# Kernel optimization log

Hardware: AMD Instinct MI355X
Metric: run time of the kernel (lower is better)

Reference implementation:

```python
import jax, jax.numpy as jnp
import numpy as np

B, N, T_OBS, N_HEAD, D = 4, 2048, 8, 4, 16  # D = t_obs*2 = in/out feat of GAT
S, NSAMP = 2, 20
OUT_DIM = S * NSAMP  # 40
SEG = 64  # pedestrians per scene -> 32 scenes, block-diagonal mask


def _xavier(key, shape, gain=1.414):
    fan_in, fan_out = shape[-2], shape[-1]
    a = gain * np.sqrt(6.0 / (fan_in + fan_out))
    return jax.random.uniform(key, shape, jnp.float32, -a, a)


def setup_inputs() -> dict:
    key = jax.random.key(0)
    ks = jax.random.split(key, 12)
    x = jax.random.normal(ks[0], (B, N, T_OBS, 2), jnp.float32)
    # block-diagonal scene mask: 32 scenes of 64 peds each
    scene_id = jnp.arange(N) // SEG
    mask = (scene_id[:, None] == scene_id[None, :]).astype(jnp.float32)
    w = _xavier(ks[1], (N_HEAD, D, D))
    a_src = _xavier(ks[2], (N_HEAD, D, 1))
    a_dst = _xavier(ks[3], (N_HEAD, D, 1))
    bias = jnp.zeros((D,), jnp.float32)
    # MLP dims: (16,) + (16, 64) + (40,)
    W1 = _xavier(ks[4], (D, 16), gain=1.0)
    b1 = jnp.zeros((16,), jnp.float32)
    W2 = _xavier(ks[5], (16, 64), gain=1.0)
    b2 = jnp.zeros((64,), jnp.float32)
    W3 = _xavier(ks[6], (64, OUT_DIM), gain=1.0)
    b3 = jnp.zeros((OUT_DIM,), jnp.float32)
    return {"x": x, "mask": mask, "w": w, "a_src": a_src, "a_dst": a_dst,
            "bias": bias, "W1": W1, "b1": b1, "W2": W2, "b2": b2, "W3": W3, "b3": b3}


def reference(x, mask, w, a_src, a_dst, bias, W1, b1, W2, b2, W3, b3):
    b, n = x.shape[0], x.shape[1]
    node = x.reshape(b, n, -1)                       # (B, N, 16)
    # GAT
    hp = jnp.einsum('bni,hio->bhno', node, w)        # (B, H, N, D)
    attn_src = jnp.einsum('bhno,hoe->bhne', hp, a_src)[..., 0]  # (B, H, N)
    attn_dst = jnp.einsum('bhno,hoe->bhne', hp, a_dst)[..., 0]  # (B, H, N)
    attn = attn_src[:, :, :, None] * attn_dst[:, :, None, :]    # (B, H, N, N)
    attn = jnp.where(attn >= 0, attn, 0.2 * attn)    # leaky_relu(0.2)
    attn = jax.nn.softmax(attn, axis=-1)             # softmax over full row
    attn = attn * mask                                # mask AFTER softmax (as in source)
    out = jnp.einsum('bhnm,bhmo->bno', attn, hp) + bias
    out = out + hp.sum(axis=1)                        # skip connection
    # MLP head: activation applied BEFORE each Linear (per source), dropout disabled
    y = jax.nn.relu(out) @ W1 + b1
    y = jax.nn.relu(y) @ W2 + b2
    y = jax.nn.relu(y) @ W3 + b3
    y = y.reshape(b, n, NSAMP, -1)[..., 0:S]          # (B, N, 20, 2)
    return jnp.clip(jax.nn.sigmoid(y), 0.01, 0.99)
```

## Files before the change

kernel.cpp:

```cpp
#include <hip/hip_runtime.h>
#include <math.h>

#define L2E 1.4426950408889634f

#if defined(__has_builtin)
#if __has_builtin(__builtin_amdgcn_exp2f)
#define EXP2F(x) __builtin_amdgcn_exp2f(x)
#else
#define EXP2F(x) exp2f(x)
#endif
#else
#define EXP2F(x) exp2f(x)
#endif

#define WS_HP   0
#define WS_S    524288
#define WS_LP   557056
#define WS_LN   589824
#define WS_NME  622592
#define WS_DINV 655360

__global__ __launch_bounds__(128, 4) void k_proj(
    const float* __restrict__ x, const float* __restrict__ w,
    const float* __restrict__ a_src, const float* __restrict__ a_dst,
    float* __restrict__ ws)
{
    __shared__ float w_s[256], as_s[16], ad_s[16];
    int t = threadIdx.x;
    int bh = blockIdx.x >> 5, tile = blockIdx.x & 31;
    int h = bh & 3, b = bh >> 2;
    int nl = t >> 1, half = t & 1;
    int n = tile * 64 + nl;
    w_s[t] = w[h * 256 + t];
    w_s[128 + t] = w[h * 256 + 128 + t];
    if (t < 16) { as_s[t] = a_src[h * 16 + t]; ad_s[t] = a_dst[h * 16 + t]; }
    __syncthreads();

    const float4* xp = (const float4*)(x + ((size_t)b * 2048 + n) * 16);
    float4 x0 = xp[0], x1 = xp[1], x2 = xp[2], x3 = xp[3];
    float nv[16] = {x0.x,x0.y,x0.z,x0.w, x1.x,x1.y,x1.z,x1.w,
                    x2.x,x2.y,x2.z,x2.w, x3.x,x3.y,x3.z,x3.w};
    int ob = half * 8;
    float acc[8];
    #pragma unroll
    for (int o = 0; o < 8; ++o) acc[o] = 0.f;
    #pragma unroll
    for (int i = 0; i < 16; ++i) {
        float ni = nv[i];
        #pragma unroll
        for (int o = 0; o < 8; ++o) acc[o] = fmaf(ni, w_s[i * 16 + ob + o], acc[o]);
    }
    float sv = 0.f, dv = 0.f;
    #pragma unroll
    for (int o = 0; o < 8; ++o) {
        sv = fmaf(acc[o], as_s[ob + o], sv);
        dv = fmaf(acc[o], ad_s[ob + o], dv);
    }
    sv += __shfl_xor(sv, 1);
    dv += __shfl_xor(dv, 1);
    float4* hp4 = (float4*)(ws + WS_HP) + ((size_t)bh * 2048 + n) * 4 + half * 2;
    hp4[0] = make_float4(acc[0], acc[1], acc[2], acc[3]);
    hp4[1] = make_float4(acc[4], acc[5], acc[6], acc[7]);
    if (half == 0) {
        size_t o = (size_t)bh * 2048 + n;
        ws[WS_S + o]  = sv;
        ws[WS_LP + o] = fmaxf(dv, 0.2f * dv);
        ws[WS_LN + o] = fminf(dv, 0.2f * dv);
    }
}

__global__ __launch_bounds__(256, 8) void k_denom(float* __restrict__ ws)
{
    __shared__ __align__(16) float img[4232];
    __shared__ float redmx[4], redmn[4];
    int t = threadIdx.x;
    int bh = blockIdx.x >> 7, tile = blockIdx.x & 127;

    float mx = -3.4e38f, mn = 3.4e38f;
    {
        const float4* glp = (const float4*)(ws + WS_LP) + bh * 512;
        const float4* gln = (const float4*)(ws + WS_LN) + bh * 512;
        #pragma unroll
        for (int k = 0; k < 2; ++k) {
            int j4 = t + k * 256;
            float4 v = glp[j4];
            int pp = j4 >> 5, wi = j4 & 31;
            *(float4*)&img[(pp * 33 + wi) * 4] = v;
            mx = fmaxf(mx, fmaxf(fmaxf(v.x, v.y), fmaxf(v.z, v.w)));
        }
        #pragma unroll
        for (int k = 0; k < 2; ++k) {
            int j4 = t + k * 256;
            float4 v = gln[j4];
            int pp = j4 >> 5, wi = j4 & 31;
            *(float4*)&img[2120 + (pp * 33 + wi) * 4] = v;
            mn = fminf(mn, fminf(fminf(v.x, v.y), fminf(v.z, v.w)));
        }
    }
    #pragma unroll
    for (int off = 32; off >= 1; off >>= 1) {
        mx = fmaxf(mx, __shfl_xor(mx, off));
        mn = fminf(mn, __shfl_xor(mn, off));
    }
    if ((t & 63) == 0) { redmx[t >> 6] = mx; redmn[t >> 6] = mn; }
    __syncthreads();
    float LPmax = fmaxf(fmaxf(redmx[0], redmx[1]), fmaxf(redmx[2], redmx[3]));
    float LNmin = fminf(fminf(redmn[0], redmn[1]), fminf(redmn[2], redmn[3]));

    int r = t >> 4, p = t & 15;
    int grow = tile * 16 + r;
    size_t base = (size_t)bh * 2048 + grow;
    float s = ws[WS_S + base];
    float me_nat = (s >= 0.f) ? s * LPmax : s * LNmin;
    float nme = -me_nat * L2E;
    float sL = s * L2E;
    const float4* ib = (const float4*)&img[(s >= 0.f) ? 0 : 2120] + p * 33;
    float a0 = 0.f, a1 = 0.f, a2 = 0.f, a3 = 0.f;
    #pragma unroll 8
    for (int c4 = 0; c4 < 32; ++c4) {
        float4 v = ib[c4];
        a0 += EXP2F(fmaf(sL, v.x, nme));
        a1 += EXP2F(fmaf(sL, v.y, nme));
        a2 += EXP2F(fmaf(sL, v.z, nme));
        a3 += EXP2F(fmaf(sL, v.w, nme));
    }
    float acc = (a0 + a1) + (a2 + a3);
    acc += __shfl_xor(acc, 1);
    acc += __shfl_xor(acc, 2);
    acc += __shfl_xor(acc, 4);
    acc += __shfl_xor(acc, 8);
    if (p == 0) {
        ws[WS_NME  + base] = nme;
        ws[WS_DINV + base] = 1.0f / acc;
    }
}

__global__ __launch_bounds__(512, 4) void k_scene(
    const float* __restrict__ ws, const float* __restrict__ bias,
    const float* __restrict__ W1, const float* __restrict__ b1,
    const float* __restrict__ W2, const float* __restrict__ b2,
    const float* __restrict__ W3, const float* __restrict__ b3,
    float* __restrict__ out)
{
    __shared__ __align__(16) float RC[5120];
    __shared__ __align__(16) float RB[1024];
    __shared__ __align__(16) float wS[3960];
    __shared__ __align__(16) float imgS[2][4][64];
    __shared__ float feat[16][17];

    const int t = threadIdx.x;
    const int b  = blockIdx.x >> 7;
    const int sc = (blockIdx.x >> 2) & 31;
    const int qt = blockIdx.x & 3;
    const int n0 = sc * 64;
    const int r0 = n0 + qt * 16;

    {
        const float4* gh = (const float4*)(ws + WS_HP);
        #pragma unroll
        for (int rep = 0; rep < 2; ++rep) {
            int u = t + rep * 512;
            int h = u >> 8, m = (u >> 2) & 63, q = u & 3;
            float4 v = gh[((size_t)(b * 4 + h) * 2048 + n0 + m) * 4 + q];
            *(float4*)&RC[(h * 64 + m) * 20 + q * 4] = v;
        }
        if (t < 128) {
            int which = t >> 6, h = (t >> 4) & 3, j4 = t & 15;
            const float4* g = (const float4*)(ws + (which ? WS_LN : WS_LP))
                              + ((size_t)(b * 4 + h) * 2048 + n0) / 4 + j4;
            *(float4*)&imgS[which][h][j4 * 4] = *g;
        }
        #pragma unroll
        for (int rep = 0; rep < 5; ++rep) wS[1360 + t + rep * 512] = W3[t + rep * 512];
        wS[272 + t] = W2[t];
        if (t < 512) wS[784 + t] = W2[512 + t];
        if (t < 256) wS[t] = W1[t];
        if (t < 16) wS[256 + t] = b1[t];
        else if (t >= 32 && t < 96) wS[1296 + (t - 32)] = b2[t - 32];
        else if (t >= 96 && t < 136) wS[3920 + (t - 96)] = b3[t - 96];
    }
    __syncthreads();

    {
        int wv = t >> 6, L = t & 63;
        int h = wv >> 1;
        int kk = (wv & 1) * 8 + (L >> 3);
        int p = L & 7;
        size_t base = (size_t)(b * 4 + h) * 2048 + r0 + kk;
        float s   = ws[WS_S + base];
        float nme = ws[WS_NME + base];
        float inv = ws[WS_DINV + base];
        float sL = s * L2E;
        const float* imgp = &imgS[(s >= 0.f) ? 0 : 1][h][0];
        float a[16];
        #pragma unroll
        for (int i = 0; i < 16; ++i) a[i] = 0.f;
        #pragma unroll
        for (int c = 0; c < 8; ++c) {
            int m = c * 8 + p;
            float e = fmaf(sL, imgp[m], nme);
            float pr = EXP2F(e) * inv;
            const float4* hr = ((const float4*)RC) + (h * 64 + m) * 5;
            float4 h0 = hr[0], h1 = hr[1], h2 = hr[2], h3 = hr[3];
            a[0]  = fmaf(pr, h0.x, a[0]);  a[1]  = fmaf(pr, h0.y, a[1]);
            a[2]  = fmaf(pr, h0.z, a[2]);  a[3]  = fmaf(pr, h0.w, a[3]);
            a[4]  = fmaf(pr, h1.x, a[4]);  a[5]  = fmaf(pr, h1.y, a[5]);
            a[6]  = fmaf(pr, h1.z, a[6]);  a[7]  = fmaf(pr, h1.w, a[7]);
            a[8]  = fmaf(pr, h2.x, a[8]);  a[9]  = fmaf(pr, h2.y, a[9]);
            a[10] = fmaf(pr, h2.z, a[10]); a[11] = fmaf(pr, h2.w, a[11]);
            a[12] = fmaf(pr, h3.x, a[12]); a[13] = fmaf(pr, h3.y, a[13]);
            a[14] = fmaf(pr, h3.z, a[14]); a[15] = fmaf(pr, h3.w, a[15]);
        }
        #pragma unroll
        for (int i = 0; i < 16; ++i) {
            a[i] += __shfl_xor(a[i], 1);
            a[i] += __shfl_xor(a[i], 2);
            a[i] += __shfl_xor(a[i], 4);
        }
        if (p == 0) {
            float* po = &RB[(h * 16 + kk) * 16];
            #pragma unroll
            for (int i = 0; i < 16; ++i) po[i] = a[i];
        }
    }
    __syncthreads();

    if (t < 256) {
        int k = t >> 4, i = t & 15;
        float v = bias[i];
        #pragma unroll
        for (int h = 0; h < 4; ++h)
            v += RB[(h * 16 + k) * 16 + i] + RC[(h * 64 + qt * 16 + k) * 20 + i];
        feat[k][i] = v;
    }
    __syncthreads();

    if (t < 256) {
        int k = t >> 4, j = t & 15;
        float acc = wS[256 + j];
        #pragma unroll
        for (int i = 0; i < 16; ++i)
            acc = fmaf(fmaxf(feat[k][i], 0.f), wS[i * 16 + j], acc);
        RC[k * 17 + j] = acc;
    }
    __syncthreads();

    {
        int k = t >> 5, g = t & 31;
        float acc0 = wS[1296 + g * 2], acc1 = wS[1296 + g * 2 + 1];
        #pragma unroll
        for (int j = 0; j < 16; ++j) {
            float r = fmaxf(RC[k * 17 + j], 0.f);
            acc0 = fmaf(r, wS[272 + j * 64 + g * 2], acc0);
            acc1 = fmaf(r, wS[272 + j * 64 + g * 2 + 1], acc1);
        }
        RC[544 + k * 65 + g * 2]     = acc0;
        RC[544 + k * 65 + g * 2 + 1] = acc1;
    }
    __syncthreads();

    for (int idx = t; idx < 640; idx += 512) {
        int k = idx / 40, c = idx % 40;
        float acc = wS[3920 + c];
        #pragma unroll 8
        for (int q = 0; q < 64; ++q)
            acc = fmaf(fmaxf(RC[544 + k * 65 + q], 0.f), wS[1360 + q * 40 + c], acc);
        float v = 1.0f / (1.0f + EXP2F(-acc * L2E));
        v = fminf(fmaxf(v, 0.01f), 0.99f);
        out[((size_t)(b * 2048) + r0 + k) * 40 + c] = v;
    }
}

extern "C" void kernel_launch(void* const* d_in, const int* in_sizes, int n_in,
                              void* d_out, int out_size, void* d_ws, size_t ws_size,
                              hipStream_t stream) {
    (void)in_sizes; (void)n_in; (void)out_size; (void)ws_size;
    const float* x     = (const float*)d_in[0];
    const float* w     = (const float*)d_in[2];
    const float* a_src = (const float*)d_in[3];
    const float* a_dst = (const float*)d_in[4];
    const float* bias  = (const float*)d_in[5];
    const float* W1    = (const float*)d_in[6];
    const float* b1    = (const float*)d_in[7];
    const float* W2    = (const float*)d_in[8];
    const float* b2    = (const float*)d_in[9];
    const float* W3    = (const float*)d_in[10];
    const float* b3    = (const float*)d_in[11];
    float* ws   = (float*)d_ws;
    float* outp = (float*)d_out;

    hipLaunchKernelGGL(k_proj, dim3(512), dim3(128), 0, stream,
                       x, w, a_src, a_dst, ws);
    hipLaunchKernelGGL(k_denom, dim3(2048), dim3(256), 0, stream, ws);
    hipLaunchKernelGGL(k_scene, dim3(512), dim3(512), 0, stream,
                       ws, bias, W1, b1, W2, b2, W3, b3, outp);
}
```

Measured before the change: 32.05 us.

## Fold attention vectors into projection and recompute hp inside scene kernel

k_proj now precomputes w·a_src and w·a_dst per head, so each node's attention scalars come from a 16-wide dot product on x and the full hp projection is no longer written to workspace. k_scene loads the scene's x rows and w into shared memory and recomputes hp locally before the aggregation. This removes the 512K-float hp round trip through global memory and shrinks the projection kernel's grid. In exchange k_scene does redundant projection arithmetic in each of its four quarter-tiles and uses more shared memory, which may lower occupancy.

```diff
diff --git a/kernel.cpp b/kernel.cpp
--- a/kernel.cpp
+++ b/kernel.cpp
@@ -13,60 +13,48 @@
 #define EXP2F(x) exp2f(x)
 #endif
 
-#define WS_HP   0
-#define WS_S    524288
-#define WS_LP   557056
-#define WS_LN   589824
-#define WS_NME  622592
-#define WS_DINV 655360
-
-__global__ __launch_bounds__(128, 4) void k_proj(
+#define WS_S    0
+#define WS_LP   32768
+#define WS_LN   65536
+#define WS_NME  98304
+#define WS_DINV 131072
+
+__global__ __launch_bounds__(256) void k_proj(
     const float* __restrict__ x, const float* __restrict__ w,
     const float* __restrict__ a_src, const float* __restrict__ a_dst,
     float* __restrict__ ws)
 {
-    __shared__ float w_s[256], as_s[16], ad_s[16];
+    __shared__ float w_s[256], cs_s[16], cd_s[16];
     int t = threadIdx.x;
-    int bh = blockIdx.x >> 5, tile = blockIdx.x & 31;
+    int bh = blockIdx.x >> 3, tile = blockIdx.x & 7;
     int h = bh & 3, b = bh >> 2;
-    int nl = t >> 1, half = t & 1;
-    int n = tile * 64 + nl;
     w_s[t] = w[h * 256 + t];
-    w_s[128 + t] = w[h * 256 + 128 + t];
-    if (t < 16) { as_s[t] = a_src[h * 16 + t]; ad_s[t] = a_dst[h * 16 + t]; }
-    __syncthreads();
-
+    __syncthreads();
+    if (t < 32) {
+        int which = t >> 4, i = t & 15;
+        const float* av = which ? (a_dst + h * 16) : (a_src + h * 16);
+        float acc = 0.f;
+        #pragma unroll
+        for (int o = 0; o < 16; ++o) acc = fmaf(w_s[i * 16 + o], av[o], acc);
+        (which ? cd_s : cs_s)[i] = acc;
+    }
+    __syncthreads();
+
+    int n = tile * 256 + t;
     const float4* xp = (const float4*)(x + ((size_t)b * 2048 + n) * 16);
     float4 x0 = xp[0], x1 = xp[1], x2 = xp[2], x3 = xp[3];
-    float nv[16] = {x0.x,x0.y,x0.z,x0.w, x1.x,x1.y,x1.z,x1.w,
+    float xr[16] = {x0.x,x0.y,x0.z,x0.w, x1.x,x1.y,x1.z,x1.w,
                     x2.x,x2.y,x2.z,x2.w, x3.x,x3.y,x3.z,x3.w};
-    int ob = half * 8;
-    float acc[8];
-    #pragma unroll
-    for (int o = 0; o < 8; ++o) acc[o] = 0.f;
+    float sv = 0.f, dv = 0.f;
     #pragma unroll
     for (int i = 0; i < 16; ++i) {
-        float ni = nv[i];
-        #pragma unroll
-        for (int o = 0; o < 8; ++o) acc[o] = fmaf(ni, w_s[i * 16 + ob + o], acc[o]);
-    }
-    float sv = 0.f, dv = 0.f;
-    #pragma unroll
-    for (int o = 0; o < 8; ++o) {
-        sv = fmaf(acc[o], as_s[ob + o], sv);
-        dv = fmaf(acc[o], ad_s[ob + o], dv);
-    }
-    sv += __shfl_xor(sv, 1);
-    dv += __shfl_xor(dv, 1);
-    float4* hp4 = (float4*)(ws + WS_HP) + ((size_t)bh * 2048 + n) * 4 + half * 2;
-    hp4[0] = make_float4(acc[0], acc[1], acc[2], acc[3]);
-    hp4[1] = make_float4(acc[4], acc[5], acc[6], acc[7]);
-    if (half == 0) {
-        size_t o = (size_t)bh * 2048 + n;
-        ws[WS_S + o]  = sv;
-        ws[WS_LP + o] = fmaxf(dv, 0.2f * dv);
-        ws[WS_LN + o] = fminf(dv, 0.2f * dv);
-    }
+        sv = fmaf(xr[i], cs_s[i], sv);
+        dv = fmaf(xr[i], cd_s[i], dv);
+    }
+    size_t o = (size_t)bh * 2048 + n;
+    ws[WS_S + o]  = sv;
+    ws[WS_LP + o] = fmaxf(dv, 0.2f * dv);
+    ws[WS_LN + o] = fminf(dv, 0.2f * dv);
 }
 
 __global__ __launch_bounds__(256, 8) void k_denom(float* __restrict__ ws)
@@ -136,6 +124,7 @@
 }
 
 __global__ __launch_bounds__(512, 4) void k_scene(
+    const float* __restrict__ x, const float* __restrict__ w,
     const float* __restrict__ ws, const float* __restrict__ bias,
     const float* __restrict__ W1, const float* __restrict__ b1,
     const float* __restrict__ W2, const float* __restrict__ b2,
@@ -146,6 +135,8 @@
     __shared__ __align__(16) float RB[1024];
     __shared__ __align__(16) float wS[3960];
     __shared__ __align__(16) float imgS[2][4][64];
+    __shared__ __align__(16) float xsS[1088];
+    __shared__ __align__(16) float wA[1024];
     __shared__ float feat[16][17];
 
     const int t = threadIdx.x;
@@ -156,14 +147,12 @@
     const int r0 = n0 + qt * 16;
 
     {
-        const float4* gh = (const float4*)(ws + WS_HP);
-        #pragma unroll
-        for (int rep = 0; rep < 2; ++rep) {
-            int u = t + rep * 512;
-            int h = u >> 8, m = (u >> 2) & 63, q = u & 3;
-            float4 v = gh[((size_t)(b * 4 + h) * 2048 + n0 + m) * 4 + q];
-            *(float4*)&RC[(h * 64 + m) * 20 + q * 4] = v;
-        }
+        const float* xb = x + ((size_t)b * 2048 + n0) * 16;
+        int u0 = t, u1 = t + 512;
+        xsS[(u0 >> 4) * 17 + (u0 & 15)] = xb[u0];
+        xsS[(u1 >> 4) * 17 + (u1 & 15)] = xb[u1];
+        wA[t] = w[t];
+        wA[512 + t] = w[512 + t];
         if (t < 128) {
             int which = t >> 6, h = (t >> 4) & 3, j4 = t & 15;
             const float4* g = (const float4*)(ws + (which ? WS_LN : WS_LP))
@@ -173,11 +162,29 @@
         #pragma unroll
         for (int rep = 0; rep < 5; ++rep) wS[1360 + t + rep * 512] = W3[t + rep * 512];
         wS[272 + t] = W2[t];
-        if (t < 512) wS[784 + t] = W2[512 + t];
+        wS[784 + t] = W2[512 + t];
         if (t < 256) wS[t] = W1[t];
         if (t < 16) wS[256 + t] = b1[t];
         else if (t >= 32 && t < 96) wS[1296 + (t - 32)] = b2[t - 32];
         else if (t >= 96 && t < 136) wS[3920 + (t - 96)] = b3[t - 96];
+    }
+    __syncthreads();
+
+    #pragma unroll
+    for (int rep = 0; rep < 2; ++rep) {
+        int u = t + rep * 512;
+        int h = u >> 8, m = (u >> 2) & 63, oq = u & 3;
+        float a0 = 0.f, a1 = 0.f, a2 = 0.f, a3 = 0.f;
+        #pragma unroll
+        for (int i = 0; i < 16; ++i) {
+            float xv = xsS[m * 17 + i];
+            const float* wr = &wA[h * 256 + i * 16 + oq * 4];
+            a0 = fmaf(xv, wr[0], a0);
+            a1 = fmaf(xv, wr[1], a1);
+            a2 = fmaf(xv, wr[2], a2);
+            a3 = fmaf(xv, wr[3], a3);
+        }
+        *(float4*)&RC[(h * 64 + m) * 20 + oq * 4] = make_float4(a0, a1, a2, a3);
     }
     __syncthreads();
 
@@ -289,9 +296,9 @@
     float* ws   = (float*)d_ws;
     float* outp = (float*)d_out;
 
-    hipLaunchKernelGGL(k_proj, dim3(512), dim3(128), 0, stream,
+    hipLaunchKernelGGL(k_proj, dim3(128), dim3(256), 0, stream,
                        x, w, a_src, a_dst, ws);
     hipLaunchKernelGGL(k_denom, dim3(2048), dim3(256), 0, stream, ws);
     hipLaunchKernelGGL(k_scene, dim3(512), dim3(512), 0, stream,
-                       ws, bias, W1, b1, W2, b2, W3, b3, outp);
+                       x, w, ws, bias, W1, b1, W2, b2, W3, b3, outp);
 }
```

Result: no change. 31.95 us (-0.3%).
